# Performance work log

Measured on AMD Instinct MI355X. Metric: run time of the kernel, lower is better.

Reference implementation:

```python
import jax, jax.numpy as jnp
import numpy as np

B, C, H, W = 8, 64, 64, 64
HID = 256  # hidden width of gate_strength_fc


def _init_params(key):
    ks = jax.random.split(key, 12)
    s = 0.05
    p = {}
    p['Wq'] = jax.random.normal(ks[0], (C, C), jnp.float32) * s
    p['bq'] = jnp.zeros((C,), jnp.float32)
    p['Wk'] = jax.random.normal(ks[1], (C, C), jnp.float32) * s
    p['bk'] = jnp.zeros((C,), jnp.float32)
    p['Wv'] = jax.random.normal(ks[2], (C, C), jnp.float32) * s
    p['bv'] = jnp.zeros((C,), jnp.float32)
    p['Wg'] = jax.random.normal(ks[3], (C, C), jnp.float32) * s
    p['bg'] = jnp.zeros((C,), jnp.float32)
    p['W1'] = jax.random.normal(ks[4], (HID, C), jnp.float32) * s
    p['b1'] = jnp.zeros((HID,), jnp.float32)
    p['W2'] = jax.random.normal(ks[5], (1, HID), jnp.float32) * s
    p['b2'] = jnp.zeros((1,), jnp.float32)
    return p


def setup_inputs() -> dict:
    key = jax.random.key(0)
    k0, k1, k2, kp = jax.random.split(key, 4)
    x = jax.random.normal(k0, (B, C, H, W), jnp.float32)
    # torch.rand(...) > 0.8 dropout-style mask, precomputed as 0/1 float for determinism
    mask = (jax.random.uniform(k1, (B, 1, H, W), jnp.float32) > 0.8).astype(jnp.float32)
    use_entropy_gate = jax.random.bernoulli(k2, 0.5, (B,))
    inp = {'x': x, 'mask': mask, 'use_entropy_gate': use_entropy_gate}
    inp.update(_init_params(kp))
    return inp


def _conv1x1(w, b, t):
    # 1x1 conv == per-pixel matmul over channels
    return jnp.einsum('oc,bchw->bohw', w, t) + b[None, :, None, None]


def reference(x, mask, use_entropy_gate, Wq, bq, Wk, bk, Wv, bv, Wg, bg, W1, b1, W2, b2):
    b_, c_, h_, w_ = x.shape
    n = h_ * w_
    masked_x = x * mask
    q = _conv1x1(Wq, bq, masked_x).reshape(b_, c_, n).transpose(0, 2, 1)  # [B,N,C]
    k = _conv1x1(Wk, bk, masked_x).reshape(b_, c_, n)                      # [B,C,N]
    v = _conv1x1(Wv, bv, x).reshape(b_, c_, n)                             # [B,C,N]
    attn = jax.nn.softmax(jnp.einsum('bnc,bcm->bnm', q, k), axis=-1)       # [B,N,N]
    out = jnp.einsum('bcn,bmn->bcm', v, attn).reshape(b_, c_, h_, w_)
    hidden = jax.nn.relu(_conv1x1(W1, b1, x))
    gate_strength = jax.nn.sigmoid(_conv1x1(W2, b2, hidden))               # [B,1,H,W]
    gate = jax.nn.sigmoid(_conv1x1(Wg, bg, x))                             # [B,C,H,W]
    flag = use_entropy_gate[:, None, None, None]
    return jnp.where(flag, out * gate * gate_strength, x)
```

## Files before the change

### kernel.cpp

```cpp
#include <hip/hip_runtime.h>
#include <hip/hip_bf16.h>
#include <math.h>

namespace {
constexpr int kB = 8;
constexpr int kC = 64;
constexpr int kN = 4096;
constexpr int kCap = 1280;
constexpr int kQS = 1312;
constexpr int kSplit = 4;
constexpr long kSeg = (long)kB * kC * kN;
typedef __attribute__((ext_vector_type(8))) short short8;
typedef __attribute__((ext_vector_type(4))) float f32x4;
}

__global__ __launch_bounds__(256) void prep_compact_kernel(
    const float* __restrict__ mask,
    const float* __restrict__ Wq, const float* __restrict__ Wk,
    const float* __restrict__ Wv, const float* __restrict__ Wg,
    const float* __restrict__ W1,
    const float* __restrict__ bq, const float* __restrict__ bk,
    const float* __restrict__ bv, const float* __restrict__ bg,
    const float* __restrict__ b1,
    int* __restrict__ p2i, int* __restrict__ cnt,
    __hip_bfloat16* __restrict__ Wfrag, float* __restrict__ bias_all) {
  const int t = threadIdx.x;
  if (blockIdx.x < kB) {
    const int b = blockIdx.x;
    __shared__ int sc_[256];
    const int base = b * kN + t * 16;
    unsigned flags = 0;
    int c16 = 0;
#pragma unroll
    for (int u = 0; u < 16; ++u) {
      const int a = (mask[base + u] != 0.f) ? 1 : 0;
      flags |= (unsigned)a << u;
      c16 += a;
    }
    sc_[t] = c16;
    __syncthreads();
    for (int off = 1; off < 256; off <<= 1) {
      const int v = (t >= off) ? sc_[t - off] : 0;
      __syncthreads();
      sc_[t] += v;
      __syncthreads();
    }
    int rank = sc_[t] - c16;
#pragma unroll
    for (int u = 0; u < 16; ++u) {
      const int n = t * 16 + u;
      const int a = (flags >> u) & 1;
      int r = -1;
      if (a) {
        if (rank < kCap) r = rank;
        rank += 1;
      }
      p2i[b * kN + n] = r;
    }
    if (t == 255) cnt[b] = sc_[255];
    return;
  }
  const int e = (blockIdx.x - kB) * 256 + t;
  const int mt = e >> 7;
  const int ks = (e >> 6) & 1;
  const int lane = e & 63;
  const int m = mt * 16 + (lane & 15);
  const int k0 = ks * 32 + (lane >> 4) * 8;
  const float* Wsrc;
  int row;
  if (m < 64)       { Wsrc = Wq; row = m; }
  else if (m < 128) { Wsrc = Wk; row = m - 64; }
  else if (m < 192) { Wsrc = Wv; row = m - 128; }
  else if (m < 256) { Wsrc = Wg; row = m - 192; }
  else              { Wsrc = W1; row = m - 256; }
#pragma unroll
  for (int j = 0; j < 8; ++j)
    Wfrag[(long)e * 8 + j] = __float2bfloat16(Wsrc[row * kC + k0 + j]);
  if (e < 512) {
    float bb;
    if (e < 64)       bb = bq[e];
    else if (e < 128) bb = bk[e - 64];
    else if (e < 192) bb = bv[e - 128];
    else if (e < 256) bb = bg[e - 192];
    else              bb = b1[e - 256];
    bias_all[e] = bb;
  }
}

__global__ __launch_bounds__(256) void dense_kernel(
    const float* __restrict__ x, const float* __restrict__ mask,
    const int* __restrict__ flag, const int* __restrict__ p2i,
    const __hip_bfloat16* __restrict__ Wfrag, const float* __restrict__ bias_all,
    const float* __restrict__ W2, const float* __restrict__ b2,
    __hip_bfloat16* __restrict__ G, float* __restrict__ GS,
    __hip_bfloat16* __restrict__ Qa, __hip_bfloat16* __restrict__ Ka,
    __hip_bfloat16* __restrict__ VaT, float* __restrict__ Sq,
    float* __restrict__ xmsP) {
  const int b = blockIdx.y;
  if (!flag[b]) return;
  const int n0 = blockIdx.x * 64;
  const int t = threadIdx.x;

  __shared__ __hip_bfloat16 sX[64][72];
  __shared__ float sB[512];
  __shared__ float sW2[256];
  {
    const int c = t >> 2;
    const int nn = (t & 3) * 16;
    const float* xp = x + (long)b * kC * kN + (long)c * kN + n0 + nn;
#pragma unroll
    for (int u = 0; u < 16; ++u) sX[nn + u][c] = __float2bfloat16(xp[u]);
  }
  sB[t] = bias_all[t];
  sB[t + 256] = bias_all[t + 256];
  sW2[t] = W2[t];
  __syncthreads();

  const int w = t >> 6;
  const int lane = t & 63;
  const int col = lane & 15;
  const int quad = lane >> 4;
  const int nl = w * 16 + col;
  const int n = n0 + nl;

  const short8 bfr0 = *(const short8*)&sX[nl][quad * 8];
  const short8 bfr1 = *(const short8*)&sX[nl][32 + quad * 8];

  const int i_act = p2i[b * kN + n];
  const float b2v = b2[0];

  float gs_acc = 0.f;
  float sq_acc = 0.f;
  for (int mt = 0; mt < 32; ++mt) {
    f32x4 acc = {0.f, 0.f, 0.f, 0.f};
    const short8 a0 = *(const short8*)(Wfrag + (((long)(mt * 2 + 0) * 64 + lane) * 8));
    const short8 a1 = *(const short8*)(Wfrag + (((long)(mt * 2 + 1) * 64 + lane) * 8));
    acc = __builtin_amdgcn_mfma_f32_16x16x32_bf16(a0, bfr0, acc, 0, 0, 0);
    acc = __builtin_amdgcn_mfma_f32_16x16x32_bf16(a1, bfr1, acc, 0, 0, 0);
    const int rbase = mt * 16 + quad * 4;
    if (mt < 4) {
      if (i_act >= 0) {
#pragma unroll
        for (int g = 0; g < 4; ++g) {
          const int r = rbase + g;
          const float qv = acc[g] + sB[r];
          Qa[((long)b * kCap + i_act) * kC + r] = __float2bfloat16(qv);
          sq_acc += qv * sB[64 + r];
        }
      }
    } else if (mt < 8) {
      if (i_act >= 0) {
#pragma unroll
        for (int g = 0; g < 4; ++g) {
          const int r = rbase + g;
          Ka[((long)b * kCap + i_act) * kC + (r - 64)] = __float2bfloat16(acc[g] + sB[r]);
        }
      }
    } else if (mt < 12) {
      if (i_act >= 0) {
#pragma unroll
        for (int g = 0; g < 4; ++g) {
          const int r = rbase + g;
          VaT[((long)b * kC + (r - 128)) * kCap + i_act] =
              __float2bfloat16(acc[g] + sB[r]);
        }
      }
    } else if (mt < 16) {
#pragma unroll
      for (int g = 0; g < 4; ++g) {
        const int r = rbase + g;
        const float gv = 1.f / (1.f + __expf(-(acc[g] + sB[r])));
        G[((long)b * kC + (r - 192)) * kN + n] = __float2bfloat16(gv);
      }
    } else {
#pragma unroll
      for (int g = 0; g < 4; ++g) {
        const int r = rbase + g;
        gs_acc += sW2[r - 256] * fmaxf(acc[g] + sB[r], 0.f);
      }
    }
  }
  gs_acc += __shfl_xor(gs_acc, 16);
  gs_acc += __shfl_xor(gs_acc, 32);
  sq_acc += __shfl_xor(sq_acc, 16);
  sq_acc += __shfl_xor(sq_acc, 32);
  if (quad == 0) {
    GS[(long)b * kN + n] = 1.f / (1.f + __expf(-(gs_acc + b2v)));
    if (i_act >= 0) Sq[(long)b * kCap + i_act] = sq_acc;
  }

  {
    const int c = t >> 2;
    const int g4 = t & 3;
    const float* mp = mask + (long)b * kN + n0 + g4 * 16;
    float s = 0.f;
#pragma unroll
    for (int u = 0; u < 16; ++u)
      if (mp[u] == 0.f) s += __bfloat162float(sX[g4 * 16 + u][c]);
    s += __shfl_xor(s, 1);
    s += __shfl_xor(s, 2);
    if (g4 == 0) xmsP[((long)b * 64 + blockIdx.x) * kC + c] = s;
  }
}

__global__ __launch_bounds__(64) void attn_act_kernel(
    const __hip_bfloat16* __restrict__ Qa, const __hip_bfloat16* __restrict__ Ka,
    const __hip_bfloat16* __restrict__ VaT,
    const int* __restrict__ cnt, const int* __restrict__ flag,
    const float* __restrict__ bq, const float* __restrict__ bk,
    const float* __restrict__ bv, const float* __restrict__ Wv,
    const float* __restrict__ xmsP,
    float* __restrict__ Pm, float* __restrict__ Pl,
    __hip_bfloat16* __restrict__ Po,
    float* __restrict__ Vsum, float* __restrict__ s0M) {
  const int b = blockIdx.z;
  if (!flag[b]) return;
  const int lane = threadIdx.x;

  __shared__ __hip_bfloat16 sP[16][40];
  __shared__ float sxm[kC];

  if (blockIdx.x == kQS / 16) {
    if (blockIdx.y != 0) return;
    float acc = 0.f;
    for (int k = 0; k < 64; ++k) acc += xmsP[((long)b * 64 + k) * kC + lane];
    sxm[lane] = acc;
    __syncthreads();
    float v = 0.f;
#pragma unroll
    for (int o = 0; o < kC; ++o) v += Wv[lane * kC + o] * sxm[o];
    Vsum[b * kC + lane] = v + (float)(kN - cnt[b]) * bv[lane];
    float pp = bq[lane] * bk[lane];
#pragma unroll
    for (int d = 1; d < 64; d <<= 1) pp += __shfl_xor(pp, d);
    if (lane == 0) s0M[0] = pp;
    return;
  }

  const int cc = min(cnt[b], kCap);
  const int ccq = cc + 1;
  const int q0 = blockIdx.x * 16;
  if (q0 >= ccq) return;
  const int s = blockIdx.y;
  const int col = lane & 15;
  const int quad = lane >> 4;
  const int gq = q0 + col;

  const int nT = (cc + 31) >> 5;
  const int tq = (nT + kSplit - 1) / kSplit;
  const int t0 = s * tq;
  const int t1 = min(t0 + tq, nT);
  const long pb = ((long)b * kSplit + s) * kQS + gq;

  if (t0 >= t1) {
    if (gq < ccq) {
      if (quad == 0) { Pm[pb] = -3e38f; Pl[pb] = 0.f; }
#pragma unroll
      for (int ct = 0; ct < 4; ++ct)
#pragma unroll
        for (int g = 0; g < 4; ++g)
          Po[pb * kC + ct * 16 + quad * 4 + g] = __float2bfloat16(0.f);
    }
    return;
  }

  short8 qf0, qf1;
  if (gq == cc) {
#pragma unroll
    for (int j = 0; j < 8; ++j) {
      ((__hip_bfloat16*)&qf0)[j] = __float2bfloat16(bq[quad * 8 + j]);
      ((__hip_bfloat16*)&qf1)[j] = __float2bfloat16(bq[32 + quad * 8 + j]);
    }
  } else {
    const int qrow = (gq < cc) ? gq : (cc - 1);
    const __hip_bfloat16* qr = Qa + ((long)b * kCap + qrow) * kC + quad * 8;
    qf0 = *(const short8*)(qr);
    qf1 = *(const short8*)(qr + 32);
  }

  float Mi = -3e38f, Li = 0.f;
  f32x4 oacc[4];
#pragma unroll
  for (int ct = 0; ct < 4; ++ct) oacc[ct] = (f32x4){0.f, 0.f, 0.f, 0.f};

  for (int kt = t0; kt < t1; ++kt) {
    const int i0 = kt * 32;
    const int kr0 = min(i0 + col, cc - 1);
    const int kr1 = min(i0 + 16 + col, cc - 1);
    const __hip_bfloat16* kp0 = Ka + ((long)b * kCap + kr0) * kC + quad * 8;
    const __hip_bfloat16* kp1 = Ka + ((long)b * kCap + kr1) * kC + quad * 8;
    const short8 kf00 = *(const short8*)(kp0);
    const short8 kf01 = *(const short8*)(kp0 + 32);
    const short8 kf10 = *(const short8*)(kp1);
    const short8 kf11 = *(const short8*)(kp1 + 32);

    f32x4 sa0 = {0.f, 0.f, 0.f, 0.f}, sa1 = {0.f, 0.f, 0.f, 0.f};
    sa0 = __builtin_amdgcn_mfma_f32_16x16x32_bf16(kf00, qf0, sa0, 0, 0, 0);
    sa0 = __builtin_amdgcn_mfma_f32_16x16x32_bf16(kf01, qf1, sa0, 0, 0, 0);
    sa1 = __builtin_amdgcn_mfma_f32_16x16x32_bf16(kf10, qf0, sa1, 0, 0, 0);
    sa1 = __builtin_amdgcn_mfma_f32_16x16x32_bf16(kf11, qf1, sa1, 0, 0, 0);

    float sc[8];
#pragma unroll
    for (int g = 0; g < 4; ++g) {
      sc[g]     = (i0 + quad * 4 + g < cc)      ? sa0[g] : -3e38f;
      sc[4 + g] = (i0 + 16 + quad * 4 + g < cc) ? sa1[g] : -3e38f;
    }
    float lm = sc[0];
#pragma unroll
    for (int u = 1; u < 8; ++u) lm = fmaxf(lm, sc[u]);
    lm = fmaxf(lm, __shfl_xor(lm, 16));
    lm = fmaxf(lm, __shfl_xor(lm, 32));
    const float newM = fmaxf(Mi, lm);
    const float alpha = __expf(Mi - newM);
    float p[8], ps = 0.f;
#pragma unroll
    for (int u = 0; u < 8; ++u) { p[u] = __expf(sc[u] - newM); ps += p[u]; }
    ps += __shfl_xor(ps, 16);
    ps += __shfl_xor(ps, 32);
    Li = Li * alpha + ps;
    Mi = newM;

#pragma unroll
    for (int g = 0; g < 4; ++g) {
      sP[col][quad * 4 + g] = __float2bfloat16(p[g]);
      sP[col][16 + quad * 4 + g] = __float2bfloat16(p[4 + g]);
    }
    __syncthreads();
    const short8 pf = *(const short8*)&sP[col][quad * 8];

#pragma unroll
    for (int ct = 0; ct < 4; ++ct)
#pragma unroll
      for (int g = 0; g < 4; ++g) oacc[ct][g] *= alpha;
#pragma unroll
    for (int ct = 0; ct < 4; ++ct) {
      const short8 vf = *(const short8*)(
          VaT + ((long)b * kC + ct * 16 + col) * kCap + i0 + quad * 8);
      oacc[ct] = __builtin_amdgcn_mfma_f32_16x16x32_bf16(vf, pf, oacc[ct], 0, 0, 0);
    }
    __syncthreads();
  }

  if (gq < ccq) {
    if (quad == 0) { Pm[pb] = Mi; Pl[pb] = Li; }
#pragma unroll
    for (int ct = 0; ct < 4; ++ct)
#pragma unroll
      for (int g = 0; g < 4; ++g)
        Po[pb * kC + ct * 16 + quad * 4 + g] = __float2bfloat16(oacc[ct][g]);
  }
}

__global__ __launch_bounds__(256) void epilogue_kernel(
    const float* __restrict__ x, const int* __restrict__ flag,
    const int* __restrict__ p2i, const int* __restrict__ cnt,
    const float* __restrict__ Pm, const float* __restrict__ Pl,
    const __hip_bfloat16* __restrict__ Po, const float* __restrict__ Sq,
    const float* __restrict__ s0M, const float* __restrict__ Vsum,
    const __hip_bfloat16* __restrict__ G, const float* __restrict__ GS,
    float* __restrict__ out) {
  const int b = blockIdx.z;
  const int cg = blockIdx.y;
  const int n = blockIdx.x * 256 + threadIdx.x;
  const int t = threadIdx.x;
  const long bbase = (long)b * kC * kN + n;
  if (!flag[b]) {
#pragma unroll
    for (int u = 0; u < 16; ++u) {
      const long a = bbase + (long)(cg * 16 + u) * kN;
      out[a] = x[a];
    }
    return;
  }
  const int cTrue = cnt[b];
  const int cc = min(cTrue, kCap);
  const float multF = (float)(kN - cTrue);

  __shared__ float sFac[5];
  __shared__ float sOM16[16];
  __shared__ float sVs[16];
  if (t == 0) {
    const float s0 = s0M[0];
    float mar[kSplit], lar[kSplit];
    float M = s0;
#pragma unroll
    for (int s = 0; s < kSplit; ++s) {
      const long pbs = ((long)b * kSplit + s) * kQS + cc;
      mar[s] = Pm[pbs];
      lar[s] = Pl[pbs];
      M = fmaxf(M, mar[s]);
    }
    const float p0 = __expf(s0 - M);
    float L = multF * p0;
    float wgt[kSplit];
#pragma unroll
    for (int s = 0; s < kSplit; ++s) { wgt[s] = __expf(mar[s] - M); L += lar[s] * wgt[s]; }
    const float invL = 1.f / L;
#pragma unroll
    for (int s = 0; s < kSplit; ++s) sFac[s] = wgt[s] * invL;
    sFac[4] = p0 * invL;
  }
  if (t < 16) sVs[t] = Vsum[b * kC + cg * 16 + t];
  __syncthreads();
  if (t < 16) {
    const int c = cg * 16 + t;
    float o = sFac[4] * sVs[t];
#pragma unroll
    for (int s = 0; s < kSplit; ++s)
      o += sFac[s] * __bfloat162float(Po[(((long)b * kSplit + s) * kQS + cc) * kC + c]);
    sOM16[t] = o;
  }
  __syncthreads();

  const float gsv = GS[(long)b * kN + n];
  const int i = p2i[b * kN + n];
  float fac[kSplit], facP = 0.f;
  if (i >= 0) {
    const float s0 = Sq[(long)b * kCap + i];
    float mar[kSplit], lar[kSplit];
    float M = s0;
#pragma unroll
    for (int s = 0; s < kSplit; ++s) {
      const long pbs = ((long)b * kSplit + s) * kQS + i;
      mar[s] = Pm[pbs];
      lar[s] = Pl[pbs];
      M = fmaxf(M, mar[s]);
    }
    const float p0 = __expf(s0 - M);
    float L = multF * p0;
#pragma unroll
    for (int s = 0; s < kSplit; ++s) { fac[s] = __expf(mar[s] - M); L += lar[s] * fac[s]; }
    const float invL = 1.f / L;
#pragma unroll
    for (int s = 0; s < kSplit; ++s) fac[s] *= invL;
    facP = p0 * invL;
  }
#pragma unroll
  for (int u = 0; u < 16; ++u) {
    const int c = cg * 16 + u;
    float r;
    if (i >= 0) {
      r = facP * sVs[u];
#pragma unroll
      for (int s = 0; s < kSplit; ++s)
        r += fac[s] * __bfloat162float(Po[(((long)b * kSplit + s) * kQS + i) * kC + c]);
    } else {
      r = sOM16[u];
    }
    const long a = bbase + (long)c * kN;
    out[a] = r * __bfloat162float(G[a]) * gsv;
  }
}

extern "C" void kernel_launch(void* const* d_in, const int* in_sizes, int n_in,
                              void* d_out, int out_size, void* d_ws, size_t ws_size,
                              hipStream_t stream) {
  (void)in_sizes; (void)n_in; (void)out_size; (void)ws_size;
  const float* x    = (const float*)d_in[0];
  const float* mask = (const float*)d_in[1];
  const int*   flag = (const int*)d_in[2];
  const float* Wq = (const float*)d_in[3];
  const float* bq = (const float*)d_in[4];
  const float* Wk = (const float*)d_in[5];
  const float* bk = (const float*)d_in[6];
  const float* Wv = (const float*)d_in[7];
  const float* bv = (const float*)d_in[8];
  const float* Wg = (const float*)d_in[9];
  const float* bg = (const float*)d_in[10];
  const float* W1 = (const float*)d_in[11];
  const float* b1 = (const float*)d_in[12];
  const float* W2 = (const float*)d_in[13];
  const float* b2 = (const float*)d_in[14];
  float* out = (float*)d_out;

  char* w = (char*)d_ws;
  float* GS = (float*)w;                       w += (long)kB * kN * 4;
  __hip_bfloat16* G  = (__hip_bfloat16*)w;     w += kSeg * 2;
  __hip_bfloat16* Qa = (__hip_bfloat16*)w;     w += (long)kB * kCap * kC * 2;
  __hip_bfloat16* Ka = (__hip_bfloat16*)w;     w += (long)kB * kCap * kC * 2;
  __hip_bfloat16* VaT= (__hip_bfloat16*)w;     w += (long)kB * kC * kCap * 2;
  __hip_bfloat16* Po = (__hip_bfloat16*)w;     w += (long)kB * kSplit * kQS * kC * 2;
  float* Pm = (float*)w;                       w += (long)kB * kSplit * kQS * 4;
  float* Pl = (float*)w;                       w += (long)kB * kSplit * kQS * 4;
  float* Sq = (float*)w;                       w += (long)kB * kCap * 4;
  float* xmsP = (float*)w;                     w += (long)kB * 64 * kC * 4;
  __hip_bfloat16* Wfrag=(__hip_bfloat16*)w;    w += (long)512 * 64 * 2;
  float* bias_all = (float*)w;                 w += 512 * 4;
  int* p2i = (int*)w;                          w += (long)kB * kN * 4;
  int* cnt = (int*)w;                          w += 64;
  float* Vsum = (float*)w;                     w += kB * kC * 4;
  float* s0M  = (float*)w;                     w += 64;

  prep_compact_kernel<<<kB + 16, 256, 0, stream>>>(
      mask, Wq, Wk, Wv, Wg, W1, bq, bk, bv, bg, b1, p2i, cnt, Wfrag, bias_all);
  dim3 gd(kN / 64, kB);
  dense_kernel<<<gd, 256, 0, stream>>>(x, mask, flag, p2i, Wfrag, bias_all, W2, b2,
                                       G, GS, Qa, Ka, VaT, Sq, xmsP);
  dim3 gat(kQS / 16 + 1, kSplit, kB);
  attn_act_kernel<<<gat, 64, 0, stream>>>(Qa, Ka, VaT, cnt, flag, bq, bk, bv, Wv,
                                          xmsP, Pm, Pl, Po, Vsum, s0M);
  dim3 gep(kN / 256, 4, kB);
  epilogue_kernel<<<gep, 256, 0, stream>>>(x, flag, p2i, cnt, Pm, Pl, Po, Sq,
                                           s0M, Vsum, G, GS, out);
}
```

Before: 129.4 us.

## Fold mask compaction and weight packing into dense kernel, drop prep launch

Removes the separate prep kernel. Each dense block now computes its own prefix of active mask pixels by rescanning the mask up to its tile, then ranks pixels within the tile using a wave ballot. Weights are read as fp32 and converted to bf16 fragments inside the MFMA loop, replacing the prepacked Wfrag buffer. This saves a kernel launch and a global round trip, at the cost of redundant mask scanning (up to 4096 elements per block) and repeated per-block weight conversion.

```diff
diff --git a/kernel.cpp b/kernel.cpp
--- a/kernel.cpp
+++ b/kernel.cpp
@@ -14,96 +14,33 @@
 typedef __attribute__((ext_vector_type(4))) float f32x4;
 }
 
-__global__ __launch_bounds__(256) void prep_compact_kernel(
-    const float* __restrict__ mask,
-    const float* __restrict__ Wq, const float* __restrict__ Wk,
-    const float* __restrict__ Wv, const float* __restrict__ Wg,
-    const float* __restrict__ W1,
-    const float* __restrict__ bq, const float* __restrict__ bk,
-    const float* __restrict__ bv, const float* __restrict__ bg,
-    const float* __restrict__ b1,
-    int* __restrict__ p2i, int* __restrict__ cnt,
-    __hip_bfloat16* __restrict__ Wfrag, float* __restrict__ bias_all) {
-  const int t = threadIdx.x;
-  if (blockIdx.x < kB) {
-    const int b = blockIdx.x;
-    __shared__ int sc_[256];
-    const int base = b * kN + t * 16;
-    unsigned flags = 0;
-    int c16 = 0;
-#pragma unroll
-    for (int u = 0; u < 16; ++u) {
-      const int a = (mask[base + u] != 0.f) ? 1 : 0;
-      flags |= (unsigned)a << u;
-      c16 += a;
-    }
-    sc_[t] = c16;
-    __syncthreads();
-    for (int off = 1; off < 256; off <<= 1) {
-      const int v = (t >= off) ? sc_[t - off] : 0;
-      __syncthreads();
-      sc_[t] += v;
-      __syncthreads();
-    }
-    int rank = sc_[t] - c16;
-#pragma unroll
-    for (int u = 0; u < 16; ++u) {
-      const int n = t * 16 + u;
-      const int a = (flags >> u) & 1;
-      int r = -1;
-      if (a) {
-        if (rank < kCap) r = rank;
-        rank += 1;
-      }
-      p2i[b * kN + n] = r;
-    }
-    if (t == 255) cnt[b] = sc_[255];
-    return;
-  }
-  const int e = (blockIdx.x - kB) * 256 + t;
-  const int mt = e >> 7;
-  const int ks = (e >> 6) & 1;
-  const int lane = e & 63;
-  const int m = mt * 16 + (lane & 15);
-  const int k0 = ks * 32 + (lane >> 4) * 8;
-  const float* Wsrc;
-  int row;
-  if (m < 64)       { Wsrc = Wq; row = m; }
-  else if (m < 128) { Wsrc = Wk; row = m - 64; }
-  else if (m < 192) { Wsrc = Wv; row = m - 128; }
-  else if (m < 256) { Wsrc = Wg; row = m - 192; }
-  else              { Wsrc = W1; row = m - 256; }
-#pragma unroll
-  for (int j = 0; j < 8; ++j)
-    Wfrag[(long)e * 8 + j] = __float2bfloat16(Wsrc[row * kC + k0 + j]);
-  if (e < 512) {
-    float bb;
-    if (e < 64)       bb = bq[e];
-    else if (e < 128) bb = bk[e - 64];
-    else if (e < 192) bb = bv[e - 128];
-    else if (e < 256) bb = bg[e - 192];
-    else              bb = b1[e - 256];
-    bias_all[e] = bb;
-  }
-}
-
 __global__ __launch_bounds__(256) void dense_kernel(
     const float* __restrict__ x, const float* __restrict__ mask,
-    const int* __restrict__ flag, const int* __restrict__ p2i,
-    const __hip_bfloat16* __restrict__ Wfrag, const float* __restrict__ bias_all,
+    const int* __restrict__ flag,
+    const float* __restrict__ Wq, const float* __restrict__ bq,
+    const float* __restrict__ Wk, const float* __restrict__ bk,
+    const float* __restrict__ Wv, const float* __restrict__ bv,
+    const float* __restrict__ Wg, const float* __restrict__ bg,
+    const float* __restrict__ W1, const float* __restrict__ b1,
     const float* __restrict__ W2, const float* __restrict__ b2,
     __hip_bfloat16* __restrict__ G, float* __restrict__ GS,
     __hip_bfloat16* __restrict__ Qa, __hip_bfloat16* __restrict__ Ka,
     __hip_bfloat16* __restrict__ VaT, float* __restrict__ Sq,
-    float* __restrict__ xmsP) {
+    float* __restrict__ xmsP, int* __restrict__ p2i, int* __restrict__ cnt) {
   const int b = blockIdx.y;
   if (!flag[b]) return;
-  const int n0 = blockIdx.x * 64;
+  const int tile = blockIdx.x;
+  const int n0 = tile * 64;
   const int t = threadIdx.x;
+  const int wid = t >> 6;
+  const int lane = t & 63;
 
   __shared__ __hip_bfloat16 sX[64][72];
   __shared__ float sB[512];
   __shared__ float sW2[256];
+  __shared__ int sRed[4];
+  __shared__ int sI[64];
+
   {
     const int c = t >> 2;
     const int nn = (t & 3) * 16;
@@ -111,30 +48,52 @@
 #pragma unroll
     for (int u = 0; u < 16; ++u) sX[nn + u][c] = __float2bfloat16(xp[u]);
   }
-  sB[t] = bias_all[t];
-  sB[t + 256] = bias_all[t + 256];
+  if (t < 64) { sB[t] = bq[t]; sB[64 + t] = bk[t]; sB[128 + t] = bv[t]; sB[192 + t] = bg[t]; }
+  sB[256 + t] = b1[t];
   sW2[t] = W2[t];
+  int loc = 0;
+  for (int n = t; n < n0; n += 256) loc += (mask[b * kN + n] != 0.f) ? 1 : 0;
+#pragma unroll
+  for (int d = 1; d < 64; d <<= 1) loc += __shfl_xor(loc, d);
+  if (lane == 0) sRed[wid] = loc;
   __syncthreads();
-
-  const int w = t >> 6;
-  const int lane = t & 63;
+  const int pbase = sRed[0] + sRed[1] + sRed[2] + sRed[3];
+  if (wid == 0) {
+    const bool a = mask[b * kN + n0 + lane] != 0.f;
+    const unsigned long long bal = __ballot(a);
+    int ia = a ? (pbase + (int)__popcll(bal & ((1ULL << lane) - 1ULL))) : -1;
+    if (ia >= kCap) ia = -1;
+    sI[lane] = ia;
+    p2i[b * kN + n0 + lane] = ia;
+    if (tile == 63 && lane == 0) cnt[b] = pbase + (int)__popcll(bal);
+  }
+  __syncthreads();
+
   const int col = lane & 15;
   const int quad = lane >> 4;
-  const int nl = w * 16 + col;
+  const int nl = wid * 16 + col;
   const int n = n0 + nl;
-
   const short8 bfr0 = *(const short8*)&sX[nl][quad * 8];
   const short8 bfr1 = *(const short8*)&sX[nl][32 + quad * 8];
-
-  const int i_act = p2i[b * kN + n];
+  const int i_act = sI[nl];
   const float b2v = b2[0];
 
-  float gs_acc = 0.f;
-  float sq_acc = 0.f;
+  float gs_acc = 0.f, sq_acc = 0.f;
   for (int mt = 0; mt < 32; ++mt) {
+    const float* Wsrc; int rb0;
+    if (mt < 4)       { Wsrc = Wq; rb0 = mt * 16; }
+    else if (mt < 8)  { Wsrc = Wk; rb0 = (mt - 4) * 16; }
+    else if (mt < 12) { Wsrc = Wv; rb0 = (mt - 8) * 16; }
+    else if (mt < 16) { Wsrc = Wg; rb0 = (mt - 12) * 16; }
+    else              { Wsrc = W1; rb0 = (mt - 16) * 16; }
+    const float* wp = Wsrc + (rb0 + col) * kC + quad * 8;
+    short8 a0, a1;
+#pragma unroll
+    for (int j = 0; j < 8; ++j) {
+      ((__hip_bfloat16*)&a0)[j] = __float2bfloat16(wp[j]);
+      ((__hip_bfloat16*)&a1)[j] = __float2bfloat16(wp[32 + j]);
+    }
     f32x4 acc = {0.f, 0.f, 0.f, 0.f};
-    const short8 a0 = *(const short8*)(Wfrag + (((long)(mt * 2 + 0) * 64 + lane) * 8));
-    const short8 a1 = *(const short8*)(Wfrag + (((long)(mt * 2 + 1) * 64 + lane) * 8));
     acc = __builtin_amdgcn_mfma_f32_16x16x32_bf16(a0, bfr0, acc, 0, 0, 0);
     acc = __builtin_amdgcn_mfma_f32_16x16x32_bf16(a1, bfr1, acc, 0, 0, 0);
     const int rbase = mt * 16 + quad * 4;
@@ -188,7 +147,6 @@
     GS[(long)b * kN + n] = 1.f / (1.f + __expf(-(gs_acc + b2v)));
     if (i_act >= 0) Sq[(long)b * kCap + i_act] = sq_acc;
   }
-
   {
     const int c = t >> 2;
     const int g4 = t & 3;
@@ -199,7 +157,7 @@
       if (mp[u] == 0.f) s += __bfloat162float(sX[g4 * 16 + u][c]);
     s += __shfl_xor(s, 1);
     s += __shfl_xor(s, 2);
-    if (g4 == 0) xmsP[((long)b * 64 + blockIdx.x) * kC + c] = s;
+    if (g4 == 0) xmsP[((long)b * 64 + tile) * kC + c] = s;
   }
 }
 
@@ -485,18 +443,15 @@
   float* Pl = (float*)w;                       w += (long)kB * kSplit * kQS * 4;
   float* Sq = (float*)w;                       w += (long)kB * kCap * 4;
   float* xmsP = (float*)w;                     w += (long)kB * 64 * kC * 4;
-  __hip_bfloat16* Wfrag=(__hip_bfloat16*)w;    w += (long)512 * 64 * 2;
-  float* bias_all = (float*)w;                 w += 512 * 4;
   int* p2i = (int*)w;                          w += (long)kB * kN * 4;
   int* cnt = (int*)w;                          w += 64;
   float* Vsum = (float*)w;                     w += kB * kC * 4;
   float* s0M  = (float*)w;                     w += 64;
 
-  prep_compact_kernel<<<kB + 16, 256, 0, stream>>>(
-      mask, Wq, Wk, Wv, Wg, W1, bq, bk, bv, bg, b1, p2i, cnt, Wfrag, bias_all);
-  dim3 gd(kN / 64, kB);
-  dense_kernel<<<gd, 256, 0, stream>>>(x, mask, flag, p2i, Wfrag, bias_all, W2, b2,
-                                       G, GS, Qa, Ka, VaT, Sq, xmsP);
+  dim3 gd(64, kB);
+  dense_kernel<<<gd, 256, 0, stream>>>(x, mask, flag, Wq, bq, Wk, bk, Wv, bv,
+                                       Wg, bg, W1, b1, W2, b2,
+                                       G, GS, Qa, Ka, VaT, Sq, xmsP, p2i, cnt);
   dim3 gat(kQS / 16 + 1, kSplit, kB);
   attn_act_kernel<<<gat, 64, 0, stream>>>(Qa, Ka, VaT, cnt, flag, bq, bk, bv, Wv,
                                           xmsP, Pm, Pl, Po, Vsum, s0M);
```

Result: slower. 144.8 us (+12.0%).

## Halve attention key split count and vectorize partial-output loads in epilogue

Applied to the files above, without the earlier changes.

Reduces the flash-decoding style key split from 4 to 2, so fewer partial results are written and merged, at the cost of less parallelism in the attention kernel. The final combine kernel also hoists the per-row branch out of the channel loop and reads the 16 bf16 partial outputs per split as two 16-byte vector loads instead of scalar gathers. This lowers merge traffic and instruction count but may leave the GPU underoccupied in the split attention stage.

```diff
diff --git a/kernel.cpp b/kernel.cpp
--- a/kernel.cpp
+++ b/kernel.cpp
@@ -8,7 +8,7 @@
 constexpr int kN = 4096;
 constexpr int kCap = 1280;
 constexpr int kQS = 1312;
-constexpr int kSplit = 4;
+constexpr int kSplit = 2;
 constexpr long kSeg = (long)kB * kC * kN;
 typedef __attribute__((ext_vector_type(8))) short short8;
 typedef __attribute__((ext_vector_type(4))) float f32x4;
@@ -377,7 +377,7 @@
   const int cc = min(cTrue, kCap);
   const float multF = (float)(kN - cTrue);
 
-  __shared__ float sFac[5];
+  __shared__ float sFac[kSplit + 1];
   __shared__ float sOM16[16];
   __shared__ float sVs[16];
   if (t == 0) {
@@ -399,13 +399,13 @@
     const float invL = 1.f / L;
 #pragma unroll
     for (int s = 0; s < kSplit; ++s) sFac[s] = wgt[s] * invL;
-    sFac[4] = p0 * invL;
+    sFac[kSplit] = p0 * invL;
   }
   if (t < 16) sVs[t] = Vsum[b * kC + cg * 16 + t];
   __syncthreads();
   if (t < 16) {
     const int c = cg * 16 + t;
-    float o = sFac[4] * sVs[t];
+    float o = sFac[kSplit] * sVs[t];
 #pragma unroll
     for (int s = 0; s < kSplit; ++s)
       o += sFac[s] * __bfloat162float(Po[(((long)b * kSplit + s) * kQS + cc) * kC + c]);
@@ -415,7 +415,7 @@
 
   const float gsv = GS[(long)b * kN + n];
   const int i = p2i[b * kN + n];
-  float fac[kSplit], facP = 0.f;
+  float r16[16];
   if (i >= 0) {
     const float s0 = Sq[(long)b * kCap + i];
     float mar[kSplit], lar[kSplit];
@@ -429,27 +429,34 @@
     }
     const float p0 = __expf(s0 - M);
     float L = multF * p0;
+    float fac[kSplit];
 #pragma unroll
     for (int s = 0; s < kSplit; ++s) { fac[s] = __expf(mar[s] - M); L += lar[s] * fac[s]; }
     const float invL = 1.f / L;
-#pragma unroll
-    for (int s = 0; s < kSplit; ++s) fac[s] *= invL;
-    facP = p0 * invL;
+    const float facP = p0 * invL;
+#pragma unroll
+    for (int u = 0; u < 16; ++u) r16[u] = facP * sVs[u];
+#pragma unroll
+    for (int s = 0; s < kSplit; ++s) {
+      const float f = fac[s] * invL;
+      const __hip_bfloat16* pr =
+          Po + (((long)b * kSplit + s) * kQS + i) * kC + cg * 16;
+      const short8 po0 = *(const short8*)(pr);
+      const short8 po1 = *(const short8*)(pr + 8);
+#pragma unroll
+      for (int u = 0; u < 8; ++u) {
+        r16[u]     += f * __bfloat162float(((const __hip_bfloat16*)&po0)[u]);
+        r16[8 + u] += f * __bfloat162float(((const __hip_bfloat16*)&po1)[u]);
+      }
+    }
+  } else {
+#pragma unroll
+    for (int u = 0; u < 16; ++u) r16[u] = sOM16[u];
   }
 #pragma unroll
   for (int u = 0; u < 16; ++u) {
-    const int c = cg * 16 + u;
-    float r;
-    if (i >= 0) {
-      r = facP * sVs[u];
-#pragma unroll
-      for (int s = 0; s < kSplit; ++s)
-        r += fac[s] * __bfloat162float(Po[(((long)b * kSplit + s) * kQS + i) * kC + c]);
-    } else {
-      r = sOM16[u];
-    }
-    const long a = bbase + (long)c * kN;
-    out[a] = r * __bfloat162float(G[a]) * gsv;
+    const long a = bbase + (long)(cg * 16 + u) * kN;
+    out[a] = r16[u] * __bfloat162float(G[a]) * gsv;
   }
 }
 
```

Measured after the change: 124.7 us. -3.6%, faster.
